# Kernel optimization log

Hardware: AMD Instinct MI355X
Metric: run time of the kernel (lower is better)

Reference implementation:

```python
import jax, jax.numpy as jnp
import numpy as np

CLAMP_MIN = 1e-6
CLAMP_MAX = 1e6


def setup_inputs() -> dict:
    key = jax.random.key(0)
    k1, k2, k3, k4, k5 = jax.random.split(key, 5)
    R, F, K = 4096, 256, 8
    return {
        "x1": jax.random.normal(k1, (R, F), dtype=jnp.float32),
        "x2": jax.random.normal(k2, (R, F), dtype=jnp.float32),
        "sigmas": jax.random.normal(k3, (K,), dtype=jnp.float32) * 100.0,
        "means": jax.random.normal(k4, (K,), dtype=jnp.float32),
        "sigma_parameters": jax.random.normal(k5, (K,), dtype=jnp.float32),
    }


def reference(x1, x2, sigmas, means, sigma_parameters):
    # dist_k[i,j] = sum_f (x1[i,f] - x2[j,f] - mean_k)^2
    #            = ||x1_i - x2_j||^2 - 2*mean_k*sum_f(x1_i - x2_j) + F*mean_k^2
    # Expansion avoids materializing the R x R x F broadcast tensor.
    R, F = x1.shape
    base = (
        jnp.sum(x1 * x1, axis=1)[:, None]
        + jnp.sum(x2 * x2, axis=1)[None, :]
        - 2.0 * (x1 @ x2.T)
    )  # [R, R]
    s = jnp.sum(x1, axis=1)[:, None] - jnp.sum(x2, axis=1)[None, :]  # [R, R]

    mean = means[:, None, None]  # [K,1,1]
    dist = base[None] - 2.0 * mean * s[None] + jnp.float32(F) * mean * mean  # [K,R,R]
    dist = jnp.clip(dist, CLAMP_MIN, CLAMP_MAX)

    kernel_value = jnp.exp(-dist / (2.0 * sigmas[:, None, None] ** 2))  # [K,R,R]
    softmaxed = jax.nn.softmax(kernel_value, axis=2)  # torch softmax(dim=1) per [R,R]

    weights = 1.0 / (sigma_parameters ** 2)
    normalized_weights = jax.nn.softmax(weights)  # softmax over K
    return jnp.sum(softmaxed * normalized_weights[:, None, None], axis=0)  # [R, R]
```

## Files before the change

### kernel.cpp

```cpp
#include <hip/hip_runtime.h>
#include <cmath>

#define R 4096
#define F 256
#define NK 8

typedef _Float16 half8 __attribute__((ext_vector_type(8)));
typedef _Float16 half4v __attribute__((ext_vector_type(4)));
typedef float f32x4 __attribute__((ext_vector_type(4)));

#define LOG2E      1.4426950408889634f
#define LOG2LOG2E  0.5287663729448977f


__global__ __launch_bounds__(256) void prep_kernel(
    const float* __restrict__ x1, const float* __restrict__ x2,
    const float* __restrict__ sigmas, const float* __restrict__ means,
    const float* __restrict__ sigp,
    _Float16* __restrict__ x1h, _Float16* __restrict__ x2h,
    float* __restrict__ rA, float* __restrict__ cB,
    float* __restrict__ S, float* __restrict__ prm)
{
    const int tid  = threadIdx.x;
    const int wid  = tid >> 6;
    const int lane = tid & 63;
    const int row  = blockIdx.x * 4 + wid;

    const float* src; _Float16* dsth; int r; bool isX1;
    if (row < R) { src = x1; dsth = x1h; r = row;     isX1 = true;  }
    else         { src = x2; dsth = x2h; r = row - R; isX1 = false; }

    float4 v = ((const float4*)(src + (size_t)r * F))[lane];
    half4v h = { (_Float16)v.x, (_Float16)v.y, (_Float16)v.z, (_Float16)v.w };
    *(half4v*)(dsth + (size_t)r * F + lane * 4) = h;

    float s = v.x + v.y + v.z + v.w;
    float q = v.x * v.x + v.y * v.y + v.z * v.z + v.w * v.w;
    for (int m = 1; m < 64; m <<= 1) {
        s += __shfl_xor(s, m);
        q += __shfl_xor(q, m);
    }
    if (lane < NK) {
        int k = lane;
        float sg = sigmas[k], m = means[k];
        float c  = -LOG2E / (2.f * sg * sg);
        if (isX1) rA[k * R + r] = c * (q - 2.f * m * s + (float)F * m * m) + LOG2LOG2E;
        else      cB[k * R + r] = c * (q + 2.f * m * s);
    }

    int g = blockIdx.x * 256 + tid;
    if (g < NK * R) S[g] = 0.f;

    if (blockIdx.x == 0 && tid == 0) {
        float w[NK], mx = -1e30f;
        for (int k = 0; k < NK; ++k) { float sp = sigp[k]; w[k] = 1.f / (sp * sp); mx = fmaxf(mx, w[k]); }
        float sum = 0.f;
        for (int k = 0; k < NK; ++k) { w[k] = expf(w[k] - mx); sum += w[k]; }
        for (int k = 0; k < NK; ++k) prm[k] = w[k] / sum;
        for (int k = 0; k < NK; ++k) {
            float sg = sigmas[k];
            prm[8 + k] = LOG2E / (sg * sg);
        }
    }
}

template <int PHASE>
__global__ __launch_bounds__(256, 2) void gemm_kernel(
    const _Float16* __restrict__ Ah, const _Float16* __restrict__ Bh,
    const float* __restrict__ rA, const float* __restrict__ cB,
    const float* __restrict__ prm, float* __restrict__ S, float* __restrict__ out)
{
    constexpr int SK = 72;
    __shared__ _Float16 As[128 * SK];
    __shared__ _Float16 Bs[128 * SK];

    const int tid  = threadIdx.x;
    const int lane = tid & 63;
    const int wid  = tid >> 6;
    const int wm   = wid >> 1, wn = wid & 1;
    const int q    = lane >> 4, m16 = lane & 15;
    const int tm   = blockIdx.y, tn = blockIdx.x;

    f32x4 acc[4][4];
#pragma unroll
    for (int a = 0; a < 4; ++a)
#pragma unroll
        for (int b = 0; b < 4; ++b)
            acc[a][b] = (f32x4){0.f, 0.f, 0.f, 0.f};

    for (int k0 = 0; k0 < F; k0 += 64) {
#pragma unroll
        for (int c = 0; c < 4; ++c) {
            int idx = c * 256 + tid;
            int row = idx >> 3, c8 = (idx & 7) * 8;
            *(uint4*)&As[row * SK + c8] =
                *(const uint4*)&Ah[(size_t)(tm * 128 + row) * F + k0 + c8];
            *(uint4*)&Bs[row * SK + c8] =
                *(const uint4*)&Bh[(size_t)(tn * 128 + row) * F + k0 + c8];
        }
        __syncthreads();
#pragma unroll
        for (int s = 0; s < 2; ++s) {
            half8 a[4], b[4];
#pragma unroll
            for (int mt = 0; mt < 4; ++mt)
                a[mt] = *(const half8*)&As[(wm * 64 + mt * 16 + m16) * SK + s * 32 + q * 8];
#pragma unroll
            for (int nt = 0; nt < 4; ++nt)
                b[nt] = *(const half8*)&Bs[(wn * 64 + nt * 16 + m16) * SK + s * 32 + q * 8];
#pragma unroll
            for (int mt = 0; mt < 4; ++mt)
#pragma unroll
                for (int nt = 0; nt < 4; ++nt)
                    acc[mt][nt] = __builtin_amdgcn_mfma_f32_16x16x32_f16(
                        a[mt], b[nt], acc[mt][nt], 0, 0, 0);
        }
        __syncthreads();
    }

    float g[8], wv[8];
#pragma unroll
    for (int k = 0; k < 8; ++k) g[k] = prm[8 + k];
    if (PHASE == 1) {
#pragma unroll
        for (int k = 0; k < 8; ++k) wv[k] = prm[k];
    }

    int colg[4];
    float colQ[8][4];
#pragma unroll
    for (int nt = 0; nt < 4; ++nt) {
        colg[nt] = tn * 128 + wn * 64 + nt * 16 + m16;
#pragma unroll
        for (int k = 0; k < 8; ++k) colQ[k][nt] = cB[k * R + colg[nt]];
    }

#pragma unroll
    for (int mt = 0; mt < 4; ++mt) {
#pragma unroll
        for (int r = 0; r < 4; ++r) {
            int rowg = tm * 128 + wm * 64 + mt * 16 + q * 4 + r;
            float rAv[8];
#pragma unroll
            for (int k = 0; k < 8; ++k) rAv[k] = rA[k * R + rowg];

            if (PHASE == 0) {
#pragma unroll
                for (int k = 0; k < 8; ++k) {
                    float t = 0.f;
#pragma unroll
                    for (int nt = 0; nt < 4; ++nt) {
                        float tt = fmaf(g[k], acc[mt][nt][r], rAv[k] + colQ[k][nt]);
                        t += __builtin_amdgcn_exp2f(__builtin_amdgcn_exp2f(tt));
                    }
                    t += __shfl_xor(t, 1); t += __shfl_xor(t, 2);
                    t += __shfl_xor(t, 4); t += __shfl_xor(t, 8);
                    if (m16 == 0) atomicAdd(&S[k * R + rowg], t);
                }
            } else {
                float sv[8];
#pragma unroll
                for (int k = 0; k < 8; ++k)
                    sv[k] = wv[k] * __builtin_amdgcn_rcpf(S[k * R + rowg]);
#pragma unroll
                for (int nt = 0; nt < 4; ++nt) {
                    float d = acc[mt][nt][r];
                    float o = 0.f;
#pragma unroll
                    for (int k = 0; k < 8; ++k) {
                        float tt = fmaf(g[k], d, rAv[k] + colQ[k][nt]);
                        o = fmaf(sv[k], __builtin_amdgcn_exp2f(__builtin_amdgcn_exp2f(tt)), o);
                    }
                    __builtin_nontemporal_store(o, &out[(size_t)rowg * R + colg[nt]]);
                }
            }
        }
    }
}

extern "C" void kernel_launch(void* const* d_in, const int* in_sizes, int n_in,
                              void* d_out, int out_size, void* d_ws, size_t ws_size,
                              hipStream_t stream) {
    (void)in_sizes; (void)n_in; (void)out_size; (void)ws_size;
    const float* x1     = (const float*)d_in[0];
    const float* x2     = (const float*)d_in[1];
    const float* sigmas = (const float*)d_in[2];
    const float* means  = (const float*)d_in[3];
    const float* sigp   = (const float*)d_in[4];
    float* out = (float*)d_out;

    char* ws = (char*)d_ws;
    _Float16* x1h = (_Float16*)ws;
    _Float16* x2h = (_Float16*)(ws + 2097152);
    float* S   = (float*)(ws + 4194304);
    float* rA  = (float*)(ws + 4194304 + 131072);
    float* cB  = (float*)(ws + 4194304 + 262144);
    float* prm = (float*)(ws + 4194304 + 393216);

    prep_kernel<<<2048, 256, 0, stream>>>(x1, x2, sigmas, means, sigp,
                                          x1h, x2h, rA, cB, S, prm);
    gemm_kernel<0><<<dim3(32, 32), 256, 0, stream>>>(x1h, x2h, rA, cB, prm, S, out);
    gemm_kernel<1><<<dim3(32, 32), 256, 0, stream>>>(x1h, x2h, rA, cB, prm, S, out);
}
```

Measured before the change: 180.2 us.

## Store GEMM dot products to output buffer and finish softmax in elementwise pass

Instead of recomputing the full GEMM in a second pass, the first GEMM kernel writes the raw dot products into the output buffer while accumulating softmax denominators. A new elementwise finish kernel reads those dot products back and computes the weighted kernel sum in place. This trades a second GEMM for an extra 64MB write plus a 64MB read of the R×R matrix. The dot stores are uncoalesced scalar writes from the MFMA layout, which may cost memory bandwidth.

After: 196.1 us. +8.8%, slower.

```diff
diff --git a/kernel.cpp b/kernel.cpp
--- a/kernel.cpp
+++ b/kernel.cpp
@@ -64,11 +64,10 @@
     }
 }
 
-template <int PHASE>
-__global__ __launch_bounds__(256, 2) void gemm_kernel(
+__global__ __launch_bounds__(256, 2) void gemm0_kernel(
     const _Float16* __restrict__ Ah, const _Float16* __restrict__ Bh,
     const float* __restrict__ rA, const float* __restrict__ cB,
-    const float* __restrict__ prm, float* __restrict__ S, float* __restrict__ out)
+    const float* __restrict__ prm, float* __restrict__ S, float* __restrict__ dot)
 {
     constexpr int SK = 72;
     __shared__ _Float16 As[128 * SK];
@@ -118,13 +117,9 @@
         __syncthreads();
     }
 
-    float g[8], wv[8];
+    float g[8];
 #pragma unroll
     for (int k = 0; k < 8; ++k) g[k] = prm[8 + k];
-    if (PHASE == 1) {
-#pragma unroll
-        for (int k = 0; k < 8; ++k) wv[k] = prm[k];
-    }
 
     int colg[4];
     float colQ[8][4];
@@ -144,38 +139,62 @@
 #pragma unroll
             for (int k = 0; k < 8; ++k) rAv[k] = rA[k * R + rowg];
 
-            if (PHASE == 0) {
-#pragma unroll
-                for (int k = 0; k < 8; ++k) {
-                    float t = 0.f;
-#pragma unroll
-                    for (int nt = 0; nt < 4; ++nt) {
-                        float tt = fmaf(g[k], acc[mt][nt][r], rAv[k] + colQ[k][nt]);
-                        t += __builtin_amdgcn_exp2f(__builtin_amdgcn_exp2f(tt));
-                    }
-                    t += __shfl_xor(t, 1); t += __shfl_xor(t, 2);
-                    t += __shfl_xor(t, 4); t += __shfl_xor(t, 8);
-                    if (m16 == 0) atomicAdd(&S[k * R + rowg], t);
+#pragma unroll
+            for (int nt = 0; nt < 4; ++nt)
+                dot[(size_t)rowg * R + colg[nt]] = acc[mt][nt][r];
+
+#pragma unroll
+            for (int k = 0; k < 8; ++k) {
+                float t = 0.f;
+#pragma unroll
+                for (int nt = 0; nt < 4; ++nt) {
+                    float tt = fmaf(g[k], acc[mt][nt][r], rAv[k] + colQ[k][nt]);
+                    t += __builtin_amdgcn_exp2f(__builtin_amdgcn_exp2f(tt));
                 }
-            } else {
-                float sv[8];
-#pragma unroll
-                for (int k = 0; k < 8; ++k)
-                    sv[k] = wv[k] * __builtin_amdgcn_rcpf(S[k * R + rowg]);
-#pragma unroll
-                for (int nt = 0; nt < 4; ++nt) {
-                    float d = acc[mt][nt][r];
-                    float o = 0.f;
-#pragma unroll
-                    for (int k = 0; k < 8; ++k) {
-                        float tt = fmaf(g[k], d, rAv[k] + colQ[k][nt]);
-                        o = fmaf(sv[k], __builtin_amdgcn_exp2f(__builtin_amdgcn_exp2f(tt)), o);
-                    }
-                    __builtin_nontemporal_store(o, &out[(size_t)rowg * R + colg[nt]]);
-                }
+                t += __shfl_xor(t, 1); t += __shfl_xor(t, 2);
+                t += __shfl_xor(t, 4); t += __shfl_xor(t, 8);
+                if (m16 == 0) atomicAdd(&S[k * R + rowg], t);
             }
         }
     }
+}
+
+__global__ __launch_bounds__(256) void finish_kernel(
+    const float* __restrict__ rA, const float* __restrict__ cB,
+    const float* __restrict__ S, const float* __restrict__ prm,
+    float* __restrict__ out)
+{
+    const int b  = blockIdx.x;
+    const int i  = b >> 2;
+    const int j0 = (b & 3) * 1024 + threadIdx.x * 4;
+
+    float g[8], sA[8], sv[8];
+#pragma unroll
+    for (int k = 0; k < 8; ++k) {
+        g[k]  = prm[8 + k];
+        sA[k] = rA[k * R + i];
+        sv[k] = prm[k] * __builtin_amdgcn_rcpf(S[k * R + i]);
+    }
+
+    float4 d = *(const float4*)&out[(size_t)i * R + j0];
+    float4 o = {0.f, 0.f, 0.f, 0.f};
+#pragma unroll
+    for (int k = 0; k < 8; ++k) {
+        float4 cb = *(const float4*)&cB[k * R + j0];
+        float base = sA[k];
+        float t0 = fmaf(g[k], d.x, base + cb.x);
+        float t1 = fmaf(g[k], d.y, base + cb.y);
+        float t2 = fmaf(g[k], d.z, base + cb.z);
+        float t3 = fmaf(g[k], d.w, base + cb.w);
+        o.x = fmaf(sv[k], __builtin_amdgcn_exp2f(__builtin_amdgcn_exp2f(t0)), o.x);
+        o.y = fmaf(sv[k], __builtin_amdgcn_exp2f(__builtin_amdgcn_exp2f(t1)), o.y);
+        o.z = fmaf(sv[k], __builtin_amdgcn_exp2f(__builtin_amdgcn_exp2f(t2)), o.z);
+        o.w = fmaf(sv[k], __builtin_amdgcn_exp2f(__builtin_amdgcn_exp2f(t3)), o.w);
+    }
+    __builtin_nontemporal_store(o.x, &out[(size_t)i * R + j0 + 0]);
+    __builtin_nontemporal_store(o.y, &out[(size_t)i * R + j0 + 1]);
+    __builtin_nontemporal_store(o.z, &out[(size_t)i * R + j0 + 2]);
+    __builtin_nontemporal_store(o.w, &out[(size_t)i * R + j0 + 3]);
 }
 
 extern "C" void kernel_launch(void* const* d_in, const int* in_sizes, int n_in,
@@ -199,6 +218,6 @@
 
     prep_kernel<<<2048, 256, 0, stream>>>(x1, x2, sigmas, means, sigp,
                                           x1h, x2h, rA, cB, S, prm);
-    gemm_kernel<0><<<dim3(32, 32), 256, 0, stream>>>(x1h, x2h, rA, cB, prm, S, out);
-    gemm_kernel<1><<<dim3(32, 32), 256, 0, stream>>>(x1h, x2h, rA, cB, prm, S, out);
-}
+    gemm0_kernel<<<dim3(32, 32), 256, 0, stream>>>(x1h, x2h, rA, cB, prm, S, out);
+    finish_kernel<<<16384, 256, 0, stream>>>(rA, cB, S, prm, out);
+}
```
